# Performance work log

Measured on AMD Instinct MI355X. Metric: run time of the kernel, lower is better.

Reference implementation:

```python
import math
import jax, jax.numpy as jnp
import numpy as np

HIDDEN = 2048
N_HEAD = 32
N_KV = 8
HEAD_DIM = HIDDEN // N_HEAD  # 64
B, S = 2, 2048


def setup_inputs() -> dict:
    key = jax.random.key(0)
    ks = jax.random.split(key, 9)
    sc_h = 1.0 / math.sqrt(HIDDEN)
    return {
        "X": jax.random.normal(ks[0], (B, S, HIDDEN), jnp.float32),
        "Wq": jax.random.normal(ks[1], (HIDDEN, HIDDEN), jnp.float32) * sc_h,
        "bq": jax.random.normal(ks[2], (HIDDEN,), jnp.float32) * 0.01,
        "Wk": jax.random.normal(ks[3], (N_KV * HEAD_DIM, HIDDEN), jnp.float32) * sc_h,
        "bk": jax.random.normal(ks[4], (N_KV * HEAD_DIM,), jnp.float32) * 0.01,
        "Wv": jax.random.normal(ks[5], (N_KV * HEAD_DIM, HIDDEN), jnp.float32) * sc_h,
        "bv": jax.random.normal(ks[6], (N_KV * HEAD_DIM,), jnp.float32) * 0.01,
        "Wo": jax.random.normal(ks[7], (HIDDEN, HIDDEN), jnp.float32) * sc_h,
        "bo": jax.random.normal(ks[8], (HIDDEN,), jnp.float32) * 0.01,
    }


def reference(X, Wq, bq, Wk, bk, Wv, bv, Wo, bo):
    b, s, _ = X.shape
    g = N_HEAD // N_KV  # query heads per kv head (repeat_interleave group)
    scale = 1.0 / math.sqrt(HEAD_DIM)

    q = X @ Wq.T + bq                       # [B,S,H*D]
    k = X @ Wk.T + bk                       # [B,S,KV*D]
    v = X @ Wv.T + bv                       # [B,S,KV*D]

    # q grouped as (B, KV, g, S, D): head h = kv*g + j matches repeat_interleave on dim=1
    q = q.reshape(b, s, N_KV, g, HEAD_DIM).transpose(0, 2, 3, 1, 4)  # [B,KV,g,S,D]
    k = k.reshape(b, s, N_KV, HEAD_DIM).transpose(0, 2, 1, 3)         # [B,KV,S,D]
    v = v.reshape(b, s, N_KV, HEAD_DIM).transpose(0, 2, 1, 3)         # [B,KV,S,D]

    # scores without materializing repeated K/V: broadcast kv head over g query heads
    scores = jnp.einsum("bkgqd,bkld->bkgql", q, k) * scale            # [B,KV,g,S,S]
    weights = jax.nn.softmax(scores, axis=-1)
    out = jnp.einsum("bkgql,bkld->bkgqd", weights, v)                 # [B,KV,g,S,D]

    # replicate torch's contiguous .view(B, seq, -1) applied to the [B,H,S,D]
    # tensor WITHOUT transposing back: plain row-major reshape of (B,H,S,D).
    out = out.reshape(b, s, N_HEAD * HEAD_DIM)
    return out @ Wo.T + bo
```

## Files before the change

kernel.cpp:

```cpp
#include <hip/hip_runtime.h>

#define HIDDEN 2048
#define NHEADS 32
#define NKV    8
#define HDIM   64
#define BATCH  2
#define SEQ    2048
#define MROWS  (BATCH*SEQ)
#define NQKV   3072

#define SCALEQ 0.18033688011112042f

typedef _Float16 half8_t __attribute__((ext_vector_type(8)));
typedef _Float16 half4_t __attribute__((ext_vector_type(4)));
typedef __fp16   fp16x2_t __attribute__((ext_vector_type(2)));
typedef float    f32x4_t __attribute__((ext_vector_type(4)));

#define AS1 __attribute__((address_space(1)))
#define AS3 __attribute__((address_space(3)))

__device__ __forceinline__ void async_copy16(void* lds, const void* g) {
    __builtin_amdgcn_global_load_lds((AS1 void*)g, (AS3 void*)lds, 16, 0, 0);
}

#define PRIO1 __builtin_amdgcn_s_setprio(1)
#define PRIO0 __builtin_amdgcn_s_setprio(0)
#define BAR   __builtin_amdgcn_s_barrier()


#define QSTG_A(bi, u, kb) \
    async_copy16(&As[bi][(u)*4096 + ldst], Ag + (size_t)((u)*64) * 2048 + (kb))
#define QSTG_B(bi, u, kb) \
    async_copy16(&Bs[bi][(u)*4096 + ldst], Bg + (size_t)((u)*64) * 2048 + (kb))

__global__ __launch_bounds__(512, 4) void gemm_qkv(
    const _Float16* __restrict__ A, const _Float16* __restrict__ Bm,
    const float* __restrict__ bias, _Float16* __restrict__ Qb,
    _Float16* __restrict__ kfb, _Float16* __restrict__ vfb) {
    __shared__ _Float16 As[2][8192];
    __shared__ _Float16 Bs[2][12288];

    const int tid  = threadIdx.x;
    const int wave = tid >> 6;
    const int lane = tid & 63;
    const int quad = lane >> 4;
    const int l16  = lane & 15;
    const int wr   = wave >> 2;
    const int wc   = wave & 3;

    const int lin = (int)(blockIdx.y * gridDim.x + blockIdx.x);
    const int idx = (lin & 7) * 64 + (lin >> 3);
    const int m0  = (idx >> 4) * 128;
    const int n0  = (idx & 15) * 192;

    const int srow = tid >> 3;
    const int sg   = ((tid & 7) ^ (srow & 7)) << 3;
    const _Float16* Ag = A  + (size_t)(m0 + srow) * 2048 + sg;
    const _Float16* Bg = Bm + (size_t)(n0 + srow) * 2048 + sg;
    const int ldst = wave * 512;

    const int sk = l16 & 7;
    const int g0 = ((0 + quad) ^ sk) << 3;
    const int g1 = ((4 + quad) ^ sk) << 3;
    const int abase = wr * 4096 + l16 * 64;
    const int bbase = wc * 3072 + l16 * 64;

    f32x4_t acc[4][3] = {};

    QSTG_A(0, 0, 0);  QSTG_A(0, 1, 0);
    QSTG_B(0, 0, 0);  QSTG_B(0, 1, 0);  QSTG_B(0, 2, 0);
    QSTG_B(1, 0, 64); QSTG_B(1, 1, 64); QSTG_B(1, 2, 64);
    asm volatile("s_waitcnt vmcnt(3)" ::: "memory");
    BAR;

    for (int t = 0; t < 32; ++t) {
        const int  cur = t & 1;
        const int  kA  = (t + 1) << 6;
        const int  kB  = (t + 2) << 6;
        const bool sA  = (t + 1 < 32);
        const bool sB  = (t + 2 < 32);
        half8_t a[2][2], b[3][2];

#pragma unroll
        for (int mi = 0; mi < 2; ++mi) {
            a[mi][0] = *(const half8_t*)(&As[cur][abase + mi * 1024 + g0]);
            a[mi][1] = *(const half8_t*)(&As[cur][abase + mi * 1024 + g1]);
        }
#pragma unroll
        for (int ni = 0; ni < 3; ++ni) {
            b[ni][0] = *(const half8_t*)(&Bs[cur][bbase + ni * 1024 + g0]);
            b[ni][1] = *(const half8_t*)(&Bs[cur][bbase + ni * 1024 + g1]);
        }
        if (sA) { QSTG_A(cur ^ 1, 0, kA); QSTG_A(cur ^ 1, 1, kA); }
        BAR;
        PRIO1;
#pragma unroll
        for (int mi = 0; mi < 2; ++mi)
#pragma unroll
            for (int ni = 0; ni < 3; ++ni) {
                acc[mi][ni] = __builtin_amdgcn_mfma_f32_16x16x32_f16(a[mi][0], b[ni][0], acc[mi][ni], 0, 0, 0);
                acc[mi][ni] = __builtin_amdgcn_mfma_f32_16x16x32_f16(a[mi][1], b[ni][1], acc[mi][ni], 0, 0, 0);
            }
        PRIO0;
        BAR;
#pragma unroll
        for (int mi = 0; mi < 2; ++mi) {
            a[mi][0] = *(const half8_t*)(&As[cur][abase + (2 + mi) * 1024 + g0]);
            a[mi][1] = *(const half8_t*)(&As[cur][abase + (2 + mi) * 1024 + g1]);
        }
        if (sB) { QSTG_B(cur, 0, kB); QSTG_B(cur, 1, kB); QSTG_B(cur, 2, kB); }
        BAR;
        PRIO1;
#pragma unroll
        for (int mi = 0; mi < 2; ++mi)
#pragma unroll
            for (int ni = 0; ni < 3; ++ni) {
                acc[2 + mi][ni] = __builtin_amdgcn_mfma_f32_16x16x32_f16(a[mi][0], b[ni][0], acc[2 + mi][ni], 0, 0, 0);
                acc[2 + mi][ni] = __builtin_amdgcn_mfma_f32_16x16x32_f16(a[mi][1], b[ni][1], acc[2 + mi][ni], 0, 0, 0);
            }
        PRIO0;
        if (sB) { asm volatile("s_waitcnt vmcnt(3)" ::: "memory"); }
        else    { asm volatile("s_waitcnt vmcnt(0)" ::: "memory"); }
        BAR;
    }

#pragma unroll
    for (int ni = 0; ni < 3; ++ni) {
        const int cbase = n0 + wc * 48 + ni * 16;
        const int c  = cbase + l16;
        const float bv = bias[c];
        if (cbase < 2048) {
#pragma unroll
            for (int mi = 0; mi < 4; ++mi) {
                const int r0 = m0 + wr * 64 + mi * 16 + quad * 4;
#pragma unroll
                for (int i = 0; i < 4; ++i)
                    Qb[(size_t)(r0 + i) * HIDDEN + c] = (_Float16)(acc[mi][ni][i] + bv);
            }
        } else if (cbase < 2560) {
            const int kd = c - 2048;
            const int kvh = kd >> 6, d = kd & 63;
#pragma unroll
            for (int mi = 0; mi < 4; ++mi) {
                const int r0   = m0 + wr * 64 + mi * 16 + quad * 4;
                const int bb   = r0 >> 11;
                const int sblk = (r0 & 2047) >> 6;
                const int nt   = (r0 >> 4) & 3;
                _Float16* dst = kfb + ((size_t)(bb * 8 + kvh) * 32 + sblk) * 4096 +
                    ((nt * 2 + (d >> 5)) * 64 + ((d >> 3) & 3) * 16 + quad * 4) * 8 +
                    (d & 7);
#pragma unroll
                for (int i = 0; i < 4; ++i)
                    dst[i * 8] = (_Float16)(acc[mi][ni][i] + bv);
            }
        } else {
            const int kd = c - 2560;
            const int kvh = kd >> 6, d = kd & 63;
            const int dt = (d >> 4) & 3;
#pragma unroll
            for (int mi = 0; mi < 4; ++mi) {
                const int r0   = m0 + wr * 64 + mi * 16 + quad * 4;
                const int bb   = r0 >> 11;
                const int sblk = (r0 & 2047) >> 6;
                const int nt   = (r0 >> 4) & 3;
                half4_t h;
#pragma unroll
                for (int i = 0; i < 4; ++i) h[i] = (_Float16)(acc[mi][ni][i] + bv);
                *(half4_t*)(vfb + ((size_t)(bb * 8 + kvh) * 32 + sblk) * 4096 +
                            (nt * 2 + (dt >> 1)) * 512 + quad * 128 +
                            (d & 15) * 8 + (dt & 1) * 4) = h;
            }
        }
    }
}

#define OSTG_A(bi, u, kb) \
    async_copy16(&As[bi][(u)*4096 + ldst], Ag + (size_t)((u)*64) * 2048 + (kb))
#define OSTG_B(bi, u, kb) \
    async_copy16(&Bs[bi][(u)*4096 + ldst], Bg + (size_t)((u)*64) * 2048 + (kb))

__global__ __launch_bounds__(512, 2) void gemm_out(
    const _Float16* __restrict__ A, const _Float16* __restrict__ Bm,
    const float* __restrict__ bias, float* __restrict__ C) {
    __shared__ _Float16 As[2][8192];
    __shared__ _Float16 Bs[2][16384];

    const int tid  = threadIdx.x;
    const int wave = tid >> 6;
    const int lane = tid & 63;
    const int quad = lane >> 4;
    const int l16  = lane & 15;
    const int wr   = wave >> 2;
    const int wc   = wave & 3;

    const int lin = (int)(blockIdx.y * gridDim.x + blockIdx.x);
    const int idx = (lin & 7) * 32 + (lin >> 3);
    const int m0  = (idx >> 3) * 128;
    const int n0  = (idx & 7) * 256;

    const int srow = tid >> 3;
    const int sg   = ((tid & 7) ^ (srow & 7)) << 3;
    const _Float16* Ag = A  + (size_t)(m0 + srow) * 2048 + sg;
    const _Float16* Bg = Bm + (size_t)(n0 + srow) * 2048 + sg;
    const int ldst = wave * 512;

    const int sk = l16 & 7;
    const int g0 = ((0 + quad) ^ sk) << 3;
    const int g1 = ((4 + quad) ^ sk) << 3;
    const int abase = wr * 4096 + l16 * 64;
    const int bbase = wc * 4096 + l16 * 64;

    f32x4_t acc[4][4] = {};

    OSTG_A(0, 0, 0);  OSTG_A(0, 1, 0);
    OSTG_B(0, 0, 0);  OSTG_B(0, 1, 0);  OSTG_B(0, 2, 0);  OSTG_B(0, 3, 0);
    OSTG_B(1, 0, 64); OSTG_B(1, 1, 64); OSTG_B(1, 2, 64); OSTG_B(1, 3, 64);
    asm volatile("s_waitcnt vmcnt(4)" ::: "memory");
    BAR;

    for (int t = 0; t < 32; ++t) {
        const int  cur = t & 1;
        const int  kA  = (t + 1) << 6;
        const int  kB  = (t + 2) << 6;
        const bool sA  = (t + 1 < 32);
        const bool sB  = (t + 2 < 32);
        half8_t a[2][2], b[4][2];

#pragma unroll
        for (int mi = 0; mi < 2; ++mi) {
            a[mi][0] = *(const half8_t*)(&As[cur][abase + mi * 1024 + g0]);
            a[mi][1] = *(const half8_t*)(&As[cur][abase + mi * 1024 + g1]);
        }
#pragma unroll
        for (int ni = 0; ni < 4; ++ni) {
            b[ni][0] = *(const half8_t*)(&Bs[cur][bbase + ni * 1024 + g0]);
            b[ni][1] = *(const half8_t*)(&Bs[cur][bbase + ni * 1024 + g1]);
        }
        if (sA) { OSTG_A(cur ^ 1, 0, kA); OSTG_A(cur ^ 1, 1, kA); }
        BAR;
        PRIO1;
#pragma unroll
        for (int mi = 0; mi < 2; ++mi)
#pragma unroll
            for (int ni = 0; ni < 4; ++ni) {
                acc[mi][ni] = __builtin_amdgcn_mfma_f32_16x16x32_f16(a[mi][0], b[ni][0], acc[mi][ni], 0, 0, 0);
                acc[mi][ni] = __builtin_amdgcn_mfma_f32_16x16x32_f16(a[mi][1], b[ni][1], acc[mi][ni], 0, 0, 0);
            }
        PRIO0;
        BAR;
#pragma unroll
        for (int mi = 0; mi < 2; ++mi) {
            a[mi][0] = *(const half8_t*)(&As[cur][abase + (2 + mi) * 1024 + g0]);
            a[mi][1] = *(const half8_t*)(&As[cur][abase + (2 + mi) * 1024 + g1]);
        }
        if (sB) { OSTG_B(cur, 0, kB); OSTG_B(cur, 1, kB);
                  OSTG_B(cur, 2, kB); OSTG_B(cur, 3, kB); }
        BAR;
        PRIO1;
#pragma unroll
        for (int mi = 0; mi < 2; ++mi)
#pragma unroll
            for (int ni = 0; ni < 4; ++ni) {
                acc[2 + mi][ni] = __builtin_amdgcn_mfma_f32_16x16x32_f16(a[mi][0], b[ni][0], acc[2 + mi][ni], 0, 0, 0);
                acc[2 + mi][ni] = __builtin_amdgcn_mfma_f32_16x16x32_f16(a[mi][1], b[ni][1], acc[2 + mi][ni], 0, 0, 0);
            }
        PRIO0;
        if (sB) { asm volatile("s_waitcnt vmcnt(4)" ::: "memory"); }
        else    { asm volatile("s_waitcnt vmcnt(0)" ::: "memory"); }
        BAR;
    }

#pragma unroll
    for (int ni = 0; ni < 4; ++ni) {
        const int c = n0 + wc * 64 + ni * 16 + l16;
        const float bv = bias[c];
#pragma unroll
        for (int mi = 0; mi < 4; ++mi) {
            const int r0 = m0 + wr * 64 + mi * 16 + quad * 4;
#pragma unroll
            for (int i = 0; i < 4; ++i)
                C[(size_t)(r0 + i) * HIDDEN + c] = acc[mi][ni][i] + bv;
        }
    }
}

__global__ __launch_bounds__(512, 4) void attn_kernel(
    const _Float16* __restrict__ Qb, const _Float16* __restrict__ Kf,
    const _Float16* __restrict__ Vf, _Float16* __restrict__ ctx) {
    __shared__ _Float16 S[32768];

    const int tid  = threadIdx.x;
    const int wave = tid >> 6;
    const int lane = tid & 63;
    const int quad = lane >> 4;
    const int l16  = lane & 15;
    const int qs   = wave >> 2;
    const int wh   = wave & 3;
    const int qt  = blockIdx.x;
    const int bkv = blockIdx.y;
    const int b   = bkv >> 3;
    const int kv  = bkv & 7;
    const int h   = kv * 4 + wh;

    half8_t qa[2][2];
#pragma unroll
    for (int g = 0; g < 2; ++g) {
        const _Float16* qp = Qb +
            ((size_t)(b * SEQ + qt * 64 + qs * 32 + g * 16 + l16)) * HIDDEN +
            h * 64 + quad * 8;
        qa[g][0] = *(const half8_t*)qp;
        qa[g][1] = *(const half8_t*)(qp + 32);
    }

    f32x4_t ot[2][4] = {};
    float fl[2] = {0.f, 0.f};

    const size_t kvbase = (size_t)(b * 8 + kv) * 32 * 4096;
    const int sh = wave * 512 + lane * 8;

#pragma unroll
    for (int t = 0; t < 2; ++t) {
        async_copy16(&S[t * 4096 + wave * 512],         Kf + kvbase + (size_t)t * 4096 + sh);
        async_copy16(&S[16384 + t * 4096 + wave * 512], Vf + kvbase + (size_t)t * 4096 + sh);
    }

    for (int j = 0; j < 16; ++j) {
        __syncthreads();
        if (j < 15) {
#pragma unroll
            for (int t = 0; t < 2; ++t) {
                const int tile = 2 * j + 2 + t;
                const int slot = tile & 3;
                const size_t off = kvbase + (size_t)tile * 4096 + sh;
                async_copy16(&S[slot * 4096 + wave * 512],         Kf + off);
                async_copy16(&S[16384 + slot * 4096 + wave * 512], Vf + off);
            }
        }
#pragma unroll
        for (int tt = 0; tt < 2; ++tt) {
            const int slot = (2 * j + tt) & 3;
            const int kb = slot * 4096, vb = 16384 + slot * 4096;
#pragma unroll
            for (int nt = 0; nt < 4; ++nt) {
                const half8_t kf0 = *(const half8_t*)(&S[kb + ((nt * 2 + 0) * 64 + lane) * 8]);
                const half8_t kf1 = *(const half8_t*)(&S[kb + ((nt * 2 + 1) * 64 + lane) * 8]);
                half4_t p[2];
#pragma unroll
                for (int g = 0; g < 2; ++g) {
                    f32x4_t s = {};
                    PRIO1;
                    s = __builtin_amdgcn_mfma_f32_16x16x32_f16(kf0, qa[g][0], s, 0, 0, 0);
                    s = __builtin_amdgcn_mfma_f32_16x16x32_f16(kf1, qa[g][1], s, 0, 0, 0);
                    PRIO0;
                    const float e0 = __builtin_amdgcn_exp2f(s[0]);
                    const float e1 = __builtin_amdgcn_exp2f(s[1]);
                    const float e2 = __builtin_amdgcn_exp2f(s[2]);
                    const float e3 = __builtin_amdgcn_exp2f(s[3]);
                    fl[g] += (e0 + e1) + (e2 + e3);
                    const fp16x2_t lo = __builtin_amdgcn_cvt_pkrtz(e0, e1);
                    const fp16x2_t hi = __builtin_amdgcn_cvt_pkrtz(e2, e3);
                    half4_t pv;
                    pv[0] = (_Float16)lo[0]; pv[1] = (_Float16)lo[1];
                    pv[2] = (_Float16)hi[0]; pv[3] = (_Float16)hi[1];
                    p[g] = pv;
                }
#pragma unroll
                for (int dp = 0; dp < 2; ++dp) {
                    const half8_t vv = *(const half8_t*)(&S[vb + ((nt * 2 + dp) * 64 + lane) * 8]);
                    const half4_t vlo = {vv[0], vv[1], vv[2], vv[3]};
                    const half4_t vhi = {vv[4], vv[5], vv[6], vv[7]};
                    PRIO1;
                    ot[0][dp * 2]     = __builtin_amdgcn_mfma_f32_16x16x16f16(vlo, p[0], ot[0][dp * 2], 0, 0, 0);
                    ot[1][dp * 2]     = __builtin_amdgcn_mfma_f32_16x16x16f16(vlo, p[1], ot[1][dp * 2], 0, 0, 0);
                    ot[0][dp * 2 + 1] = __builtin_amdgcn_mfma_f32_16x16x16f16(vhi, p[0], ot[0][dp * 2 + 1], 0, 0, 0);
                    ot[1][dp * 2 + 1] = __builtin_amdgcn_mfma_f32_16x16x16f16(vhi, p[1], ot[1][dp * 2 + 1], 0, 0, 0);
                    PRIO0;
                }
            }
        }
    }

#pragma unroll
    for (int g = 0; g < 2; ++g) {
        fl[g] += __shfl_xor(fl[g], 16);
        fl[g] += __shfl_xor(fl[g], 32);
    }

    __syncthreads();
    _Float16* T = S + wave * 1152;
#pragma unroll
    for (int g = 0; g < 2; ++g) {
        const float inv = 1.f / fl[g];
#pragma unroll
        for (int dt = 0; dt < 4; ++dt) {
            half4_t hh;
#pragma unroll
            for (int r = 0; r < 4; ++r) hh[r] = (_Float16)(ot[g][dt][r] * inv);
            *(half4_t*)(T + l16 * 72 + dt * 16 + quad * 4) = hh;
        }
        __builtin_amdgcn_s_waitcnt(0);
        _Float16* cp = ctx +
            (((size_t)b * 32 + h) * SEQ + qt * 64 + qs * 32 + g * 16 + l16) * 64;
#pragma unroll
        for (int pass = 0; pass < 2; ++pass) {
            const half8_t row = *(const half8_t*)(T + l16 * 72 + pass * 32 + quad * 8);
            *(half8_t*)(cp + pass * 32 + quad * 8) = row;
        }
        __builtin_amdgcn_s_waitcnt(0);
    }
}

__device__ __forceinline__ void cast4(const float* __restrict__ s,
                                      _Float16* __restrict__ d, int i, float sc) {
    const f32x4_t v = ((const f32x4_t*)s)[i];
    half4_t h;
#pragma unroll
    for (int j = 0; j < 4; ++j) h[j] = (_Float16)(v[j] * sc);
    ((half4_t*)d)[i] = h;
}

__global__ __launch_bounds__(256) void prep(
    const float* __restrict__ X,  const float* __restrict__ Wq,
    const float* __restrict__ Wk, const float* __restrict__ Wv,
    const float* __restrict__ Wo, const float* __restrict__ bq,
    const float* __restrict__ bk, const float* __restrict__ bv,
    _Float16* __restrict__ Xh, _Float16* __restrict__ Wqkv,
    _Float16* __restrict__ Woh, float* __restrict__ bqkv) {
    const int bid = blockIdx.x, tid = threadIdx.x;
    if (bid < 8192)       cast4(X,  Xh,   bid * 256 + tid, 1.f);
    else if (bid < 12288) cast4(Wq, Wqkv, (bid - 8192) * 256 + tid, SCALEQ);
    else if (bid < 13312) cast4(Wk, Wqkv + (size_t)HIDDEN * HIDDEN, (bid - 12288) * 256 + tid, 1.f);
    else if (bid < 14336) cast4(Wv, Wqkv + (size_t)(HIDDEN + 512) * HIDDEN, (bid - 13312) * 256 + tid, 1.f);
    else if (bid < 18432) cast4(Wo, Woh,  (bid - 14336) * 256 + tid, 1.f);
    else {
        const int i = (bid - 18432) * 256 + tid;
        if (i < 2048)      bqkv[i] = bq[i] * SCALEQ;
        else if (i < 2560) bqkv[i] = bk[i - 2048];
        else if (i < 3072) bqkv[i] = bv[i - 2560];
    }
}

extern "C" void kernel_launch(void* const* d_in, const int* in_sizes, int n_in,
                              void* d_out, int out_size, void* d_ws, size_t ws_size,
                              hipStream_t stream) {
    const float* X  = (const float*)d_in[0];
    const float* Wq = (const float*)d_in[1];
    const float* bq = (const float*)d_in[2];
    const float* Wk = (const float*)d_in[3];
    const float* bk = (const float*)d_in[4];
    const float* Wv = (const float*)d_in[5];
    const float* bv = (const float*)d_in[6];
    const float* Wo = (const float*)d_in[7];
    const float* bo = (const float*)d_in[8];
    float* out = (float*)d_out;

    char* p = (char*)d_ws;
    _Float16* Xh   = (_Float16*)p; p += (size_t)MROWS * HIDDEN * 2;
    _Float16* Wqkv = (_Float16*)p; p += (size_t)NQKV * HIDDEN * 2;
    _Float16* Woh  = (_Float16*)p; p += (size_t)HIDDEN * HIDDEN * 2;
    float*    bqkv = (float*)p;    p += (size_t)NQKV * 4;
    _Float16* Qb   = (_Float16*)p; p += (size_t)MROWS * HIDDEN * 2;
    _Float16* Kfb  = (_Float16*)p; p += (size_t)16 * 32 * 4096 * 2;
    _Float16* Vfb  = (_Float16*)p; p += (size_t)16 * 32 * 4096 * 2;
    _Float16* ctx  = Xh;

    prep<<<18444, 256, 0, stream>>>(X, Wq, Wk, Wv, Wo, bq, bk, bv,
                                    Xh, Wqkv, Woh, bqkv);

    gemm_qkv<<<dim3(NQKV / 192, MROWS / 128), 512, 0, stream>>>(
        Xh, Wqkv, bqkv, Qb, Kfb, Vfb);

    attn_kernel<<<dim3(SEQ / 64, BATCH * NKV), 512, 0, stream>>>(Qb, Kfb, Vfb, ctx);

    gemm_out<<<dim3(HIDDEN / 256, MROWS / 128), 512, 0, stream>>>(
        ctx, Woh, bo, out);
}
```

Before: 311.5 us.

## Halve attention query tile per block to raise occupancy and block count

```diff
diff --git a/kernel.cpp b/kernel.cpp
--- a/kernel.cpp
+++ b/kernel.cpp
@@ -284,17 +284,17 @@
     }
 }
 
-__global__ __launch_bounds__(512, 4) void attn_kernel(
+__global__ __launch_bounds__(512, 8) void attn_kernel(
     const _Float16* __restrict__ Qb, const _Float16* __restrict__ Kf,
     const _Float16* __restrict__ Vf, _Float16* __restrict__ ctx) {
-    __shared__ _Float16 S[32768];
+    __shared__ _Float16 S[16384];
 
     const int tid  = threadIdx.x;
     const int wave = tid >> 6;
     const int lane = tid & 63;
     const int quad = lane >> 4;
     const int l16  = lane & 15;
-    const int qs   = wave >> 2;
+    const int qh   = wave >> 2;
     const int wh   = wave & 3;
     const int qt  = blockIdx.x;
     const int bkv = blockIdx.y;
@@ -302,111 +302,78 @@
     const int kv  = bkv & 7;
     const int h   = kv * 4 + wh;
 
-    half8_t qa[2][2];
-#pragma unroll
-    for (int g = 0; g < 2; ++g) {
-        const _Float16* qp = Qb +
-            ((size_t)(b * SEQ + qt * 64 + qs * 32 + g * 16 + l16)) * HIDDEN +
-            h * 64 + quad * 8;
-        qa[g][0] = *(const half8_t*)qp;
-        qa[g][1] = *(const half8_t*)(qp + 32);
-    }
-
-    f32x4_t ot[2][4] = {};
-    float fl[2] = {0.f, 0.f};
+    const _Float16* qp = Qb +
+        ((size_t)(b * SEQ + qt * 32 + qh * 16 + l16)) * HIDDEN + h * 64 + quad * 8;
+    const half8_t qa0 = *(const half8_t*)qp;
+    const half8_t qa1 = *(const half8_t*)(qp + 32);
+
+    f32x4_t ot[4] = {};
+    float fl = 0.f;
 
     const size_t kvbase = (size_t)(b * 8 + kv) * 32 * 4096;
     const int sh = wave * 512 + lane * 8;
 
-#pragma unroll
-    for (int t = 0; t < 2; ++t) {
-        async_copy16(&S[t * 4096 + wave * 512],         Kf + kvbase + (size_t)t * 4096 + sh);
-        async_copy16(&S[16384 + t * 4096 + wave * 512], Vf + kvbase + (size_t)t * 4096 + sh);
-    }
-
-    for (int j = 0; j < 16; ++j) {
+    async_copy16(&S[wave * 512],        Kf + kvbase + sh);
+    async_copy16(&S[8192 + wave * 512], Vf + kvbase + sh);
+
+    for (int kt = 0; kt < SEQ / 64; ++kt) {
         __syncthreads();
-        if (j < 15) {
-#pragma unroll
-            for (int t = 0; t < 2; ++t) {
-                const int tile = 2 * j + 2 + t;
-                const int slot = tile & 3;
-                const size_t off = kvbase + (size_t)tile * 4096 + sh;
-                async_copy16(&S[slot * 4096 + wave * 512],         Kf + off);
-                async_copy16(&S[16384 + slot * 4096 + wave * 512], Vf + off);
-            }
-        }
-#pragma unroll
-        for (int tt = 0; tt < 2; ++tt) {
-            const int slot = (2 * j + tt) & 3;
-            const int kb = slot * 4096, vb = 16384 + slot * 4096;
-#pragma unroll
-            for (int nt = 0; nt < 4; ++nt) {
-                const half8_t kf0 = *(const half8_t*)(&S[kb + ((nt * 2 + 0) * 64 + lane) * 8]);
-                const half8_t kf1 = *(const half8_t*)(&S[kb + ((nt * 2 + 1) * 64 + lane) * 8]);
-                half4_t p[2];
-#pragma unroll
-                for (int g = 0; g < 2; ++g) {
-                    f32x4_t s = {};
-                    PRIO1;
-                    s = __builtin_amdgcn_mfma_f32_16x16x32_f16(kf0, qa[g][0], s, 0, 0, 0);
-                    s = __builtin_amdgcn_mfma_f32_16x16x32_f16(kf1, qa[g][1], s, 0, 0, 0);
-                    PRIO0;
-                    const float e0 = __builtin_amdgcn_exp2f(s[0]);
-                    const float e1 = __builtin_amdgcn_exp2f(s[1]);
-                    const float e2 = __builtin_amdgcn_exp2f(s[2]);
-                    const float e3 = __builtin_amdgcn_exp2f(s[3]);
-                    fl[g] += (e0 + e1) + (e2 + e3);
-                    const fp16x2_t lo = __builtin_amdgcn_cvt_pkrtz(e0, e1);
-                    const fp16x2_t hi = __builtin_amdgcn_cvt_pkrtz(e2, e3);
-                    half4_t pv;
-                    pv[0] = (_Float16)lo[0]; pv[1] = (_Float16)lo[1];
-                    pv[2] = (_Float16)hi[0]; pv[3] = (_Float16)hi[1];
-                    p[g] = pv;
-                }
-#pragma unroll
-                for (int dp = 0; dp < 2; ++dp) {
-                    const half8_t vv = *(const half8_t*)(&S[vb + ((nt * 2 + dp) * 64 + lane) * 8]);
-                    const half4_t vlo = {vv[0], vv[1], vv[2], vv[3]};
-                    const half4_t vhi = {vv[4], vv[5], vv[6], vv[7]};
-                    PRIO1;
-                    ot[0][dp * 2]     = __builtin_amdgcn_mfma_f32_16x16x16f16(vlo, p[0], ot[0][dp * 2], 0, 0, 0);
-                    ot[1][dp * 2]     = __builtin_amdgcn_mfma_f32_16x16x16f16(vlo, p[1], ot[1][dp * 2], 0, 0, 0);
-                    ot[0][dp * 2 + 1] = __builtin_amdgcn_mfma_f32_16x16x16f16(vhi, p[0], ot[0][dp * 2 + 1], 0, 0, 0);
-                    ot[1][dp * 2 + 1] = __builtin_amdgcn_mfma_f32_16x16x16f16(vhi, p[1], ot[1][dp * 2 + 1], 0, 0, 0);
-                    PRIO0;
-                }
-            }
-        }
-    }
-
-#pragma unroll
-    for (int g = 0; g < 2; ++g) {
-        fl[g] += __shfl_xor(fl[g], 16);
-        fl[g] += __shfl_xor(fl[g], 32);
-    }
+        const int cur = kt & 1;
+        if (kt + 1 < SEQ / 64) {
+            const size_t off = kvbase + (size_t)(kt + 1) * 4096 + sh;
+            async_copy16(&S[(cur ^ 1) * 4096 + wave * 512],        Kf + off);
+            async_copy16(&S[8192 + (cur ^ 1) * 4096 + wave * 512], Vf + off);
+        }
+        const int kb = cur * 4096, vb = 8192 + cur * 4096;
+
+#pragma unroll
+        for (int nt = 0; nt < 4; ++nt) {
+            const half8_t kf0 = *(const half8_t*)(&S[kb + ((nt * 2 + 0) * 64 + lane) * 8]);
+            const half8_t kf1 = *(const half8_t*)(&S[kb + ((nt * 2 + 1) * 64 + lane) * 8]);
+            f32x4_t s = {};
+            s = __builtin_amdgcn_mfma_f32_16x16x32_f16(kf0, qa0, s, 0, 0, 0);
+            s = __builtin_amdgcn_mfma_f32_16x16x32_f16(kf1, qa1, s, 0, 0, 0);
+            const float e0 = __builtin_amdgcn_exp2f(s[0]);
+            const float e1 = __builtin_amdgcn_exp2f(s[1]);
+            const float e2 = __builtin_amdgcn_exp2f(s[2]);
+            const float e3 = __builtin_amdgcn_exp2f(s[3]);
+            fl += (e0 + e1) + (e2 + e3);
+            const fp16x2_t lo = __builtin_amdgcn_cvt_pkrtz(e0, e1);
+            const fp16x2_t hi = __builtin_amdgcn_cvt_pkrtz(e2, e3);
+            half4_t p;
+            p[0] = (_Float16)lo[0]; p[1] = (_Float16)lo[1];
+            p[2] = (_Float16)hi[0]; p[3] = (_Float16)hi[1];
+#pragma unroll
+            for (int dp = 0; dp < 2; ++dp) {
+                const half8_t vv = *(const half8_t*)(&S[vb + ((nt * 2 + dp) * 64 + lane) * 8]);
+                const half4_t vlo = {vv[0], vv[1], vv[2], vv[3]};
+                const half4_t vhi = {vv[4], vv[5], vv[6], vv[7]};
+                ot[dp * 2]     = __builtin_amdgcn_mfma_f32_16x16x16f16(vlo, p, ot[dp * 2], 0, 0, 0);
+                ot[dp * 2 + 1] = __builtin_amdgcn_mfma_f32_16x16x16f16(vhi, p, ot[dp * 2 + 1], 0, 0, 0);
+            }
+        }
+    }
+
+    fl += __shfl_xor(fl, 16);
+    fl += __shfl_xor(fl, 32);
 
     __syncthreads();
     _Float16* T = S + wave * 1152;
-#pragma unroll
-    for (int g = 0; g < 2; ++g) {
-        const float inv = 1.f / fl[g];
-#pragma unroll
-        for (int dt = 0; dt < 4; ++dt) {
-            half4_t hh;
-#pragma unroll
-            for (int r = 0; r < 4; ++r) hh[r] = (_Float16)(ot[g][dt][r] * inv);
-            *(half4_t*)(T + l16 * 72 + dt * 16 + quad * 4) = hh;
-        }
-        __builtin_amdgcn_s_waitcnt(0);
-        _Float16* cp = ctx +
-            (((size_t)b * 32 + h) * SEQ + qt * 64 + qs * 32 + g * 16 + l16) * 64;
-#pragma unroll
-        for (int pass = 0; pass < 2; ++pass) {
-            const half8_t row = *(const half8_t*)(T + l16 * 72 + pass * 32 + quad * 8);
-            *(half8_t*)(cp + pass * 32 + quad * 8) = row;
-        }
-        __builtin_amdgcn_s_waitcnt(0);
+    const float inv = 1.f / fl;
+#pragma unroll
+    for (int dt = 0; dt < 4; ++dt) {
+        half4_t hh;
+#pragma unroll
+        for (int r = 0; r < 4; ++r) hh[r] = (_Float16)(ot[dt][r] * inv);
+        *(half4_t*)(T + l16 * 72 + dt * 16 + quad * 4) = hh;
+    }
+    __builtin_amdgcn_s_waitcnt(0);
+    _Float16* cp = ctx +
+        (((size_t)b * 32 + h) * SEQ + qt * 32 + qh * 16 + l16) * 64;
+#pragma unroll
+    for (int pass = 0; pass < 2; ++pass) {
+        const half8_t row = *(const half8_t*)(T + l16 * 72 + pass * 32 + quad * 8);
+        *(half8_t*)(cp + pass * 32 + quad * 8) = row;
     }
 }
 
@@ -470,7 +437,7 @@
     gemm_qkv<<<dim3(NQKV / 192, MROWS / 128), 512, 0, stream>>>(
         Xh, Wqkv, bqkv, Qb, Kfb, Vfb);
 
-    attn_kernel<<<dim3(SEQ / 64, BATCH * NKV), 512, 0, stream>>>(Qb, Kfb, Vfb, ctx);
+    attn_kernel<<<dim3(SEQ / 32, BATCH * NKV), 512, 0, stream>>>(Qb, Kfb, Vfb, ctx);
 
     gemm_out<<<dim3(HIDDEN / 256, MROWS / 128), 512, 0, stream>>>(
         ctx, Woh, bo, out);
```

After: 320.2 us. 2.8% more time.
